# Optimization experiments

Hardware: AMD Instinct MI355X
Metric: run time of the kernel (lower is better)

## Reference

```python
import jax, jax.numpy as jnp
import numpy as np

B, N, K, H = 8, 4096, 16, 64
EPS_LN = 1e-5
EPS_STD = 1e-5


def _ln(x, g, b):
    m = jnp.mean(x, -1, keepdims=True)
    v = jnp.mean((x - m) ** 2, -1, keepdims=True)
    return (x - m) * jax.lax.rsqrt(v + EPS_LN) * g + b


def _res_block(x, W1, b1, g1, be1, W2, b2, g2, be2):
    h = jax.nn.relu(_ln(x @ W1 + b1, g1, be1))
    return jax.nn.relu(x + _ln(h @ W2 + b2, g2, be2))


def setup_inputs() -> dict:
    key = jax.random.key(0)
    ks = jax.random.split(key, 12)
    def w(k, shape, scale=0.02):
        return (jax.random.normal(k, shape) * scale).astype(jnp.float32)
    h = H
    z = jnp.zeros
    o = jnp.ones
    return dict(
        xyz=jax.random.normal(ks[0], (B, N, 3), jnp.float32),
        x=jax.random.normal(ks[1], (B, N, 3), jnp.float32),
        W_emb=w(ks[2], (3, h)), b_emb=z(h), g_emb=o(h), be_emb=z(h),
        alpha=o(h), beta=z(h),
        W_pre=w(ks[3], (2 * h, 4 * h)), b_pre=z(4 * h), g_pre=o(4 * h), be_pre=z(4 * h),
        W1a=w(ks[4], (4 * h, 8 * h)), b1a=z(8 * h), g1a=o(8 * h), be1a=z(8 * h),
        W2a=w(ks[5], (8 * h, 4 * h)), b2a=z(4 * h), g2a=o(4 * h), be2a=z(4 * h),
        W_pos=w(ks[6], (4 * h, 4 * h)), b_pos=z(4 * h), g_pos=o(4 * h), be_pos=z(4 * h),
        W1b=w(ks[7], (4 * h, 8 * h)), b1b=z(8 * h), g1b=o(8 * h), be1b=z(8 * h),
        W2b=w(ks[8], (8 * h, 4 * h)), b2b=z(4 * h), g2b=o(4 * h), be2b=z(4 * h),
        W_fin=w(ks[9], (4 * h, h)), b_fin=z(h), g_fin=o(h), be_fin=z(h),
    )


def _forward(xyz, x, W_emb, b_emb, g_emb, be_emb, alpha, beta,
             W_pre, b_pre, g_pre, be_pre,
             W1a, b1a, g1a, be1a, W2a, b2a, g2a, be2a,
             W_pos, b_pos, g_pos, be_pos,
             W1b, b1b, g1b, be1b, W2b, b2b, g2b, be2b,
             W_fin, b_fin, g_fin, be_fin):
    # embedding: Linear + LN + ReLU  -> [B, N, H]
    pts = jax.nn.relu(_ln(x @ W_emb + b_emb, g_emb, be_emb))
    # KNN over xyz (squared distances, smallest K)
    sq = jnp.sum(xyz ** 2, -1)                                   # [B, N]
    sqd = sq[:, :, None] + sq[:, None, :] - 2.0 * jnp.einsum('bnd,bmd->bnm', xyz, xyz)
    _, idx = jax.lax.top_k(-sqd, K)                              # [B, N, K]
    grouped = jax.vmap(lambda p, i: p[i])(pts, idx)              # [B, N, K, H]
    # anchor normalization: mean = center feature; std over whole per-batch flattened diff (ddof=1)
    diff = grouped - pts[:, :, None, :]
    std = jnp.std(diff.reshape(diff.shape[0], -1), axis=-1, ddof=1)[:, None, None, None]
    grouped = diff / (std + EPS_STD) * alpha + beta
    newp = jnp.concatenate(
        [grouped, jnp.broadcast_to(pts[:, :, None, :], grouped.shape)], axis=-1)  # [B, N, K, 2H]
    # pre MLP + residual block, then max-pool over K
    y = _ln(newp @ W_pre + b_pre, g_pre, be_pre)                 # [B, N, K, 4H]
    y = _res_block(y, W1a, b1a, g1a, be1a, W2a, b2a, g2a, be2a)
    y = jnp.max(y, axis=2)                                       # [B, N, 4H]
    # pos MLP + residual block, then max-pool over N
    y = _ln(y @ W_pos + b_pos, g_pos, be_pos)
    y = _res_block(y, W1b, b1b, g1b, be1b, W2b, b2b, g2b, be2b)
    y = jnp.max(y, axis=1)                                       # [B, 4H]
    return _ln(y @ W_fin + b_fin, g_fin, be_fin)                 # [B, H]


def reference(xyz, x, W_emb, b_emb, g_emb, be_emb, alpha, beta,
              W_pre, b_pre, g_pre, be_pre,
              W1a, b1a, g1a, be1a, W2a, b2a, g2a, be2a,
              W_pos, b_pos, g_pos, be_pos,
              W1b, b1b, g1b, be1b, W2b, b2b, g2b, be2b,
              W_fin, b_fin, g_fin, be_fin):
    return _forward(xyz, x, W_emb, b_emb, g_emb, be_emb, alpha, beta,
                    W_pre, b_pre, g_pre, be_pre,
                    W1a, b1a, g1a, be1a, W2a, b2a, g2a, be2a,
                    W_pos, b_pos, g_pos, be_pos,
                    W1b, b1b, g1b, be1b, W2b, b2b, g2b, be2b,
                    W_fin, b_fin, g_fin, be_fin)
```

## Files before the change

kernel.cpp:

```cpp
#include <hip/hip_runtime.h>
#include <hip/hip_bf16.h>

typedef __bf16 bf16_t;
typedef __bf16 bf16x8 __attribute__((ext_vector_type(8)));
typedef __bf16 bf16x4 __attribute__((ext_vector_type(4)));
typedef float f32x4 __attribute__((ext_vector_type(4)));
typedef unsigned long long u64;

#define LNEPS 1e-5f
#define STDEPS 1e-5f

#define PTS_OFF   0UL
#define IDX_OFF   8519680UL
#define RED_OFF   10616832UL
#define STD_OFF   (RED_OFF + 128UL)
#define WP_OFF    10617088UL
#define POOL1_OFF 11862272UL
#define POOL2_OFF 28639488UL
#define WS_NEED   28647680UL

__global__ void k_pack(const float* __restrict__ W, bf16_t* __restrict__ Wp,
                       int No, int sh, int n)
{
  int i = blockIdx.x * 256 + threadIdx.x;
  if (i >= n) return;
  int j = i & 7;
  int l = (i >> 3) & 63;
  int rest = i >> 9;
  int kc = rest & ((1 << sh) - 1);
  int t = rest >> sh;
  int k = kc * 32 + (l >> 4) * 8 + j;
  int col = t * 16 + (l & 15);
  Wp[i] = (bf16_t)W[k * No + col];
}

__global__ void k_embed(const float* __restrict__ xyz, const float* __restrict__ x,
                        const float* __restrict__ W, const float* __restrict__ bb,
                        const float* __restrict__ g, const float* __restrict__ be,
                        float* __restrict__ pts, float4* __restrict__ cand4)
{
  int p = blockIdx.x * 256 + threadIdx.x;
  float x0 = x[p * 3 + 0], x1 = x[p * 3 + 1], x2 = x[p * 3 + 2];
  float e[64];
  float s = 0.f;
  #pragma unroll
  for (int j = 0; j < 64; ++j) {
    float v = bb[j];
    v = fmaf(x0, W[j], v);
    v = fmaf(x1, W[64 + j], v);
    v = fmaf(x2, W[128 + j], v);
    e[j] = v; s += v;
  }
  float mean = s * (1.f / 64.f);
  float vs = 0.f;
  #pragma unroll
  for (int j = 0; j < 64; ++j) { float d = e[j] - mean; vs = fmaf(d, d, vs); }
  float rstd = rsqrtf(vs * (1.f / 64.f) + LNEPS);
  #pragma unroll
  for (int j = 0; j < 64; ++j)
    pts[p * 64 + j] = fmaxf(0.f, (e[j] - mean) * rstd * g[j] + be[j]);
  float z0 = xyz[p * 3 + 0], z1 = xyz[p * 3 + 1], z2 = xyz[p * 3 + 2];
  cand4[p] = make_float4(z0, z1, z2, z0 * z0 + z1 * z1 + z2 * z2);
}

__device__ __forceinline__ void insert16(u64* a, u64 key)
{
  #pragma unroll
  for (int j = 15; j >= 1; --j) {
    u64 lo = (key < a[j - 1]) ? a[j - 1] : key;
    a[j] = (key < a[j]) ? lo : a[j];
  }
  a[0] = (key < a[0]) ? key : a[0];
}

__device__ __forceinline__ void merge16(u64* a, const u64* b)
{
  u64 m[16];
  #pragma unroll
  for (int i = 0; i < 16; ++i) m[i] = (a[i] < b[15 - i]) ? a[i] : b[15 - i];
  #pragma unroll
  for (int d = 8; d >= 1; d >>= 1) {
    #pragma unroll
    for (int i = 0; i < 16; ++i) {
      if ((i & d) == 0) {
        u64 xv = m[i], yv = m[i + d];
        bool c = yv < xv;
        m[i] = c ? yv : xv;
        m[i + d] = c ? xv : yv;
      }
    }
  }
  #pragma unroll
  for (int i = 0; i < 16; ++i) a[i] = m[i];
}

__global__ __launch_bounds__(256) void k_knn(const float4* __restrict__ cand4,
                                             int* __restrict__ idx)
{
  __shared__ u64 ldsB[256 * 17];
  const int tid = threadIdx.x;
  const int l = tid & 63;
  const int w = tid >> 6;
  const int wu = __builtin_amdgcn_readfirstlane(w);
  const int b = blockIdx.x >> 6;
  const int g = blockIdx.x & 63;
  const int p = (b << 12) + (g << 6) + l;
  const float4 q = cand4[p];
  const float4* __restrict__ cbase = cand4 + (b << 12) + (wu << 10);
  const int mbase = wu << 10;
  u64 arr[16];
  const u64 KINF = ((u64)0x7F800000u << 32) | 0xFFFFFFFFu;
  #pragma unroll
  for (int j = 0; j < 16; ++j) arr[j] = KINF;
  float tf = 3.4e38f;
  int cnt = 0;
  u64* myb = &ldsB[tid * 17];

  for (int m0 = 0; m0 < 1024; m0 += 8) {
    if (__any(cnt > 8)) {
      for (int j2 = 0; j2 < cnt; ++j2) insert16(arr, myb[j2]);
      cnt = 0;
      tf = __uint_as_float((unsigned)(arr[15] >> 32));
    }
    #pragma unroll
    for (int u = 0; u < 8; ++u) {
      float4 c = cbase[m0 + u];
      float dot = q.x * c.x;
      dot = fmaf(q.y, c.y, dot);
      dot = fmaf(q.z, c.z, dot);
      float d = fmaxf(fmaf(-2.f, dot, q.w + c.w), 0.f);
      if (d < tf) {
        myb[cnt] = ((u64)__float_as_uint(d) << 32) | (unsigned)(mbase + m0 + u);
        ++cnt;
      }
    }
  }
  for (int j2 = 0; j2 < cnt; ++j2) insert16(arr, myb[j2]);

  #pragma unroll
  for (int j = 0; j < 16; ++j) myb[j] = arr[j];
  __syncthreads();
  if ((w & 1) == 0) {
    u64 brr[16];
    #pragma unroll
    for (int j = 0; j < 16; ++j) brr[j] = ldsB[((w + 1) * 64 + l) * 17 + j];
    merge16(arr, brr);
    #pragma unroll
    for (int j = 0; j < 16; ++j) myb[j] = arr[j];
  }
  __syncthreads();
  if (w == 0) {
    u64 brr[16];
    #pragma unroll
    for (int j = 0; j < 16; ++j) brr[j] = ldsB[(2 * 64 + l) * 17 + j];
    merge16(arr, brr);
    #pragma unroll
    for (int j = 0; j < 16; ++j) idx[p * 16 + j] = (int)(unsigned)(arr[j] & 0xFFFFFFFFu);
  }
}

__global__ void k_stdred(const float* __restrict__ pts, const int* __restrict__ idx,
                         double* __restrict__ red)
{
  int b = blockIdx.x >> 6, chunk = blockIdx.x & 63;
  int tid = threadIdx.x;
  int h = tid & 63;
  int r0 = chunk * 1024 + (tid >> 6);
  float s = 0.f, s2 = 0.f;
  for (int i = 0; i < 256; ++i) {
    int row = r0 + 4 * i;
    int n = row >> 4, k = row & 15;
    int ni = idx[((b << 12) + n) * 16 + k];
    float v = pts[((b << 12) + ni) * 64 + h] - pts[((b << 12) + n) * 64 + h];
    s += v; s2 = fmaf(v, v, s2);
  }
  double ds = (double)s, ds2 = (double)s2;
  #pragma unroll
  for (int m = 1; m < 64; m <<= 1) {
    ds += __shfl_xor(ds, m, 64);
    ds2 += __shfl_xor(ds2, m, 64);
  }
  __shared__ double sred[8];
  int w = tid >> 6;
  if ((tid & 63) == 0) { sred[w] = ds; sred[4 + w] = ds2; }
  __syncthreads();
  if (tid == 0) {
    atomicAdd(&red[b], sred[0] + sred[1] + sred[2] + sred[3]);
    atomicAdd(&red[8 + b], sred[4] + sred[5] + sred[6] + sred[7]);
  }
}

__global__ void k_stdfin(const double* __restrict__ red, float* __restrict__ stdv)
{
  int t = threadIdx.x;
  if (t < 8) {
    double M = 4194304.0;
    double s = red[t], s2 = red[8 + t];
    double var = (s2 - s * s / M) / (M - 1.0);
    stdv[t] = (float)sqrt(var);
  }
}

__device__ __forceinline__ bf16x4 cvt4(f32x4 v)
{
  bf16x4 o;
  o[0] = (bf16_t)v[0]; o[1] = (bf16_t)v[1]; o[2] = (bf16_t)v[2]; o[3] = (bf16_t)v[3];
  return o;
}

__device__ __forceinline__ f32x4 shflmax(f32x4 v, int m)
{
  f32x4 r;
  #pragma unroll
  for (int c = 0; c < 4; ++c) r[c] = fmaxf(v[c], __shfl_xor(v[c], m, 64));
  return r;
}

template <int NKC, int NTW>
__device__ __forceinline__ void gemm_sw(const bf16_t* __restrict__ inS, const int instride,
                                        const bf16_t* __restrict__ Wp,
                                        const int w, const int l, f32x4 (*acc)[4])
{
  const int lr = l & 15, lg = l >> 4;
  const bf16x8* __restrict__ Wf = (const bf16x8*)Wp;
  #pragma unroll
  for (int kc = 0; kc < NKC; ++kc) {
    bf16x8 af[4];
    #pragma unroll
    for (int rt = 0; rt < 4; ++rt)
      af[rt] = *(const bf16x8*)(inS + (rt * 16 + lr) * instride + kc * 32 + lg * 8);
    #pragma unroll
    for (int ct = 0; ct < NTW; ++ct) {
      bf16x8 bw = Wf[((w * NTW + ct) * NKC + kc) * 64 + l];
      #pragma unroll
      for (int rt = 0; rt < 4; ++rt)
        acc[ct][rt] = __builtin_amdgcn_mfma_f32_16x16x32_bf16(bw, af[rt], acc[ct][rt], 0, 0, 0);
    }
  }
}

template <int NTW>
__device__ __forceinline__ void add_bias_stats(f32x4 (*acc)[4], const float* __restrict__ bias,
                                               const int w, const int l,
                                               float* __restrict__ smP, float* __restrict__ sqP)
{
  const int lr = l & 15, lg = l >> 4;
  float sm[4] = {0.f, 0.f, 0.f, 0.f}, sq[4] = {0.f, 0.f, 0.f, 0.f};
  #pragma unroll
  for (int ct = 0; ct < NTW; ++ct) {
    const int t = w * NTW + ct;
    f32x4 b4 = *(const f32x4*)(bias + t * 16 + 4 * lg);
    #pragma unroll
    for (int rt = 0; rt < 4; ++rt) {
      f32x4 v = acc[ct][rt] + b4;
      acc[ct][rt] = v;
      #pragma unroll
      for (int rg = 0; rg < 4; ++rg) { sm[rt] += v[rg]; sq[rt] = fmaf(v[rg], v[rg], sq[rt]); }
    }
  }
  #pragma unroll
  for (int rt = 0; rt < 4; ++rt) {
    sm[rt] += __shfl_xor(sm[rt], 16, 64); sq[rt] += __shfl_xor(sq[rt], 16, 64);
    sm[rt] += __shfl_xor(sm[rt], 32, 64); sq[rt] += __shfl_xor(sq[rt], 32, 64);
  }
  if (lg == 0) {
    #pragma unroll
    for (int rt = 0; rt < 4; ++rt) {
      smP[w * 64 + rt * 16 + lr] = sm[rt];
      sqP[w * 64 + rt * 16 + lr] = sq[rt];
    }
  }
}

__device__ __forceinline__ void mean_rstd(const float* __restrict__ smP,
                                          const float* __restrict__ sqP,
                                          const int lr, const float invNC,
                                          float* mean, float* rstd)
{
  #pragma unroll
  for (int rt = 0; rt < 4; ++rt) {
    int row = rt * 16 + lr;
    float s = 0.f, q = 0.f;
    #pragma unroll
    for (int u = 0; u < 8; ++u) { s += smP[u * 64 + row]; q += sqP[u * 64 + row]; }
    float me = s * invNC;
    float var = q * invNC - me * me;
    mean[rt] = me; rstd[rt] = rsqrtf(var + LNEPS);
  }
}

template <int NKCIN, int INSTRIDE, int REGEL, bool KPOOL>
__global__ __launch_bounds__(512, 4) void k_mlp(
    const float* __restrict__ pts, const int* __restrict__ idxp,
    const float* __restrict__ stdv, const float* __restrict__ alpha,
    const float* __restrict__ beta, const bf16_t* __restrict__ pooled1_in,
    const bf16_t* __restrict__ Wp0, const float* __restrict__ b0,
    const float* __restrict__ g0, const float* __restrict__ be0,
    const bf16_t* __restrict__ Wp1, const float* __restrict__ b1,
    const float* __restrict__ g1, const float* __restrict__ be1,
    const bf16_t* __restrict__ Wp2, const float* __restrict__ b2,
    const float* __restrict__ g2, const float* __restrict__ be2,
    bf16_t* __restrict__ pooled1_out, unsigned* __restrict__ pooled2)
{
  __shared__ bf16_t region[REGEL];
  __shared__ float smP[8 * 64];
  __shared__ float sqP[8 * 64];
  bf16_t* inS = region;
  bf16_t* yS = region + 64 * INSTRIDE;
  bf16_t* hS = region;

  const int tid = threadIdx.x;
  const int l = tid & 63, w = tid >> 6;
  const int lr = l & 15, lg = l >> 4;
  const int p0 = blockIdx.x * (KPOOL ? 4 : 64);
  const int bb = p0 >> 12;

  {
    const int r = tid >> 3, q = tid & 7;
    if (KPOOL) {
      const float inv = 1.0f / (stdv[bb] + STDEPS);
      const int p = p0 + (r >> 4), k = r & 15;
      if (q < 4) {
        const int ni = idxp[p * 16 + k];
        const float* sn = pts + ((size_t)(bb << 12) + ni) * 64 + q * 16;
        const float* sp = pts + (size_t)p * 64 + q * 16;
        #pragma unroll
        for (int i = 0; i < 4; ++i) {
          f32x4 a = *(const f32x4*)(sn + 4 * i);
          f32x4 c = *(const f32x4*)(sp + 4 * i);
          f32x4 av = *(const f32x4*)(alpha + q * 16 + 4 * i);
          f32x4 bv = *(const f32x4*)(beta + q * 16 + 4 * i);
          f32x4 v = (a - c) * (av * inv) + bv;
          *(bf16x4*)(inS + r * INSTRIDE + q * 16 + 4 * i) = cvt4(v);
        }
      } else {
        const float* sp = pts + (size_t)p * 64 + (q - 4) * 16;
        #pragma unroll
        for (int i = 0; i < 4; ++i) {
          f32x4 c = *(const f32x4*)(sp + 4 * i);
          *(bf16x4*)(inS + r * INSTRIDE + 64 + (q - 4) * 16 + 4 * i) = cvt4(c);
        }
      }
    } else {
      #pragma unroll
      for (int j = 0; j < 4; ++j) {
        *(bf16x8*)(inS + r * INSTRIDE + q * 32 + j * 8) =
            *(const bf16x8*)(pooled1_in + (size_t)(p0 + r) * 256 + q * 32 + j * 8);
      }
    }
  }
  __syncthreads();

  bf16x4 residb[2][4];
  float mean[4], rstd[4];

  {
    f32x4 acc[2][4];
    #pragma unroll
    for (int ct = 0; ct < 2; ++ct)
      #pragma unroll
      for (int rt = 0; rt < 4; ++rt) acc[ct][rt] = {0.f, 0.f, 0.f, 0.f};
    gemm_sw<NKCIN, 2>(inS, INSTRIDE, Wp0, w, l, acc);
    add_bias_stats<2>(acc, b0, w, l, smP, sqP);
    __syncthreads();
    mean_rstd(smP, sqP, lr, 1.f / 256.f, mean, rstd);
    #pragma unroll
    for (int ct = 0; ct < 2; ++ct) {
      const int t = w * 2 + ct;
      f32x4 g4 = *(const f32x4*)(g0 + t * 16 + 4 * lg);
      f32x4 be4 = *(const f32x4*)(be0 + t * 16 + 4 * lg);
      #pragma unroll
      for (int rt = 0; rt < 4; ++rt) {
        f32x4 v;
        #pragma unroll
        for (int rg = 0; rg < 4; ++rg)
          v[rg] = (acc[ct][rt][rg] - mean[rt]) * rstd[rt] * g4[rg] + be4[rg];
        bf16x4 vb = cvt4(v);
        residb[ct][rt] = vb;
        *(bf16x4*)(yS + (rt * 16 + lr) * 264 + t * 16 + 4 * lg) = vb;
      }
    }
  }
  __syncthreads();

  {
    f32x4 acc[4][4];
    #pragma unroll
    for (int ct = 0; ct < 4; ++ct)
      #pragma unroll
      for (int rt = 0; rt < 4; ++rt) acc[ct][rt] = {0.f, 0.f, 0.f, 0.f};
    gemm_sw<8, 4>(yS, 264, Wp1, w, l, acc);
    add_bias_stats<4>(acc, b1, w, l, smP, sqP);
    __syncthreads();
    mean_rstd(smP, sqP, lr, 1.f / 512.f, mean, rstd);
    #pragma unroll
    for (int ct = 0; ct < 4; ++ct) {
      const int t = w * 4 + ct;
      f32x4 g4 = *(const f32x4*)(g1 + t * 16 + 4 * lg);
      f32x4 be4 = *(const f32x4*)(be1 + t * 16 + 4 * lg);
      #pragma unroll
      for (int rt = 0; rt < 4; ++rt) {
        f32x4 v;
        #pragma unroll
        for (int rg = 0; rg < 4; ++rg)
          v[rg] = fmaxf(0.f, (acc[ct][rt][rg] - mean[rt]) * rstd[rt] * g4[rg] + be4[rg]);
        *(bf16x4*)(hS + (rt * 16 + lr) * 520 + t * 16 + 4 * lg) = cvt4(v);
      }
    }
  }
  __syncthreads();

  {
    f32x4 acc[2][4];
    #pragma unroll
    for (int ct = 0; ct < 2; ++ct)
      #pragma unroll
      for (int rt = 0; rt < 4; ++rt) acc[ct][rt] = {0.f, 0.f, 0.f, 0.f};
    gemm_sw<16, 2>(hS, 520, Wp2, w, l, acc);
    add_bias_stats<2>(acc, b2, w, l, smP, sqP);
    __syncthreads();
    mean_rstd(smP, sqP, lr, 1.f / 256.f, mean, rstd);
    #pragma unroll
    for (int ct = 0; ct < 2; ++ct) {
      const int t = w * 2 + ct;
      f32x4 g4 = *(const f32x4*)(g2 + t * 16 + 4 * lg);
      f32x4 be4 = *(const f32x4*)(be2 + t * 16 + 4 * lg);
      f32x4 mv = {0.f, 0.f, 0.f, 0.f};
      #pragma unroll
      for (int rt = 0; rt < 4; ++rt) {
        f32x4 v;
        #pragma unroll
        for (int rg = 0; rg < 4; ++rg)
          v[rg] = fmaxf(0.f, (float)residb[ct][rt][rg] +
                             (acc[ct][rt][rg] - mean[rt]) * rstd[rt] * g4[rg] + be4[rg]);
        if (KPOOL) {
          v = shflmax(v, 1); v = shflmax(v, 2); v = shflmax(v, 4); v = shflmax(v, 8);
          if (lr == 0)
            *(bf16x4*)(pooled1_out + (size_t)(p0 + rt) * 256 + t * 16 + 4 * lg) = cvt4(v);
        } else {
          #pragma unroll
          for (int rg = 0; rg < 4; ++rg) mv[rg] = fmaxf(mv[rg], v[rg]);
        }
      }
      if (!KPOOL) {
        mv = shflmax(mv, 1); mv = shflmax(mv, 2); mv = shflmax(mv, 4); mv = shflmax(mv, 8);
        if (lr == 0) {
          #pragma unroll
          for (int rg = 0; rg < 4; ++rg)
            atomicMax(&pooled2[bb * 256 + t * 16 + 4 * lg + rg], __float_as_uint(mv[rg]));
        }
      }
    }
  }
}

__global__ void k_final(const unsigned* __restrict__ pooled2,
                        const float* __restrict__ W, const float* __restrict__ bb,
                        const float* __restrict__ g, const float* __restrict__ be,
                        float* __restrict__ out)
{
  int w = threadIdx.x >> 6;
  int l = threadIdx.x & 63;
  float acc = bb[l];
  for (int k = 0; k < 256; ++k)
    acc = fmaf(__uint_as_float(pooled2[w * 256 + k]), W[k * 64 + l], acc);
  float sm = acc, sq = acc * acc;
  #pragma unroll
  for (int m = 1; m < 64; m <<= 1) {
    sm += __shfl_xor(sm, m, 64);
    sq += __shfl_xor(sq, m, 64);
  }
  float mean = sm * (1.f / 64.f);
  float var = sq * (1.f / 64.f) - mean * mean;
  out[w * 64 + l] = (acc - mean) * rsqrtf(var + LNEPS) * g[l] + be[l];
}

extern "C" void kernel_launch(void* const* d_in, const int* in_sizes, int n_in,
                              void* d_out, int out_size, void* d_ws, size_t ws_size,
                              hipStream_t stream)
{
  if (ws_size < WS_NEED) return;
  const float* xyz = (const float*)d_in[0];
  const float* x = (const float*)d_in[1];
  const float* W_emb = (const float*)d_in[2];
  const float* b_emb = (const float*)d_in[3];
  const float* g_emb = (const float*)d_in[4];
  const float* be_emb = (const float*)d_in[5];
  const float* alpha = (const float*)d_in[6];
  const float* beta = (const float*)d_in[7];
  const float* W_pre = (const float*)d_in[8];
  const float* b_pre = (const float*)d_in[9];
  const float* g_pre = (const float*)d_in[10];
  const float* be_pre = (const float*)d_in[11];
  const float* W1a = (const float*)d_in[12];
  const float* b1a = (const float*)d_in[13];
  const float* g1a = (const float*)d_in[14];
  const float* be1a = (const float*)d_in[15];
  const float* W2a = (const float*)d_in[16];
  const float* b2a = (const float*)d_in[17];
  const float* g2a = (const float*)d_in[18];
  const float* be2a = (const float*)d_in[19];
  const float* W_pos = (const float*)d_in[20];
  const float* b_pos = (const float*)d_in[21];
  const float* g_pos = (const float*)d_in[22];
  const float* be_pos = (const float*)d_in[23];
  const float* W1b = (const float*)d_in[24];
  const float* b1b = (const float*)d_in[25];
  const float* g1b = (const float*)d_in[26];
  const float* be1b = (const float*)d_in[27];
  const float* W2b = (const float*)d_in[28];
  const float* b2b = (const float*)d_in[29];
  const float* g2b = (const float*)d_in[30];
  const float* be2b = (const float*)d_in[31];
  const float* W_fin = (const float*)d_in[32];
  const float* b_fin = (const float*)d_in[33];
  const float* g_fin = (const float*)d_in[34];
  const float* be_fin = (const float*)d_in[35];

  char* ws = (char*)d_ws;
  float* pts = (float*)(ws + PTS_OFF);
  int* idx = (int*)(ws + IDX_OFF);
  double* red = (double*)(ws + RED_OFF);
  float* stdv = (float*)(ws + STD_OFF);
  bf16_t* WpPre = (bf16_t*)(ws + WP_OFF);
  bf16_t* Wp1a = WpPre + 32768;
  bf16_t* Wp2a = Wp1a + 131072;
  bf16_t* WpPos = Wp2a + 131072;
  bf16_t* Wp1b = WpPos + 65536;
  bf16_t* Wp2b = Wp1b + 131072;
  bf16_t* pooled1 = (bf16_t*)(ws + POOL1_OFF);
  float4* cand4 = (float4*)(ws + POOL1_OFF);
  unsigned* pooled2 = (unsigned*)(ws + POOL2_OFF);

  hipMemsetAsync(ws + RED_OFF, 0, 256, stream);
  hipMemsetAsync(ws + POOL2_OFF, 0, 8192, stream);

  k_pack<<<32768 / 256, 256, 0, stream>>>(W_pre, WpPre, 256, 2, 32768);
  k_pack<<<131072 / 256, 256, 0, stream>>>(W1a, Wp1a, 512, 3, 131072);
  k_pack<<<131072 / 256, 256, 0, stream>>>(W2a, Wp2a, 256, 4, 131072);
  k_pack<<<65536 / 256, 256, 0, stream>>>(W_pos, WpPos, 256, 3, 65536);
  k_pack<<<131072 / 256, 256, 0, stream>>>(W1b, Wp1b, 512, 3, 131072);
  k_pack<<<131072 / 256, 256, 0, stream>>>(W2b, Wp2b, 256, 4, 131072);

  k_embed<<<32768 / 256, 256, 0, stream>>>(xyz, x, W_emb, b_emb, g_emb, be_emb, pts, cand4);
  k_knn<<<512, 256, 0, stream>>>(cand4, idx);
  k_stdred<<<512, 256, 0, stream>>>(pts, idx, red);
  k_stdfin<<<1, 64, 0, stream>>>(red, stdv);

  k_mlp<4, 136, 33280, true><<<8192, 512, 0, stream>>>(
      pts, idx, stdv, alpha, beta, nullptr,
      WpPre, b_pre, g_pre, be_pre,
      Wp1a, b1a, g1a, be1a,
      Wp2a, b2a, g2a, be2a,
      pooled1, nullptr);
  k_mlp<8, 264, 33792, false><<<512, 512, 0, stream>>>(
      nullptr, nullptr, nullptr, nullptr, nullptr, pooled1,
      WpPos, b_pos, g_pos, be_pos,
      Wp1b, b1b, g1b, be1b,
      Wp2b, b2b, g2b, be2b,
      nullptr, pooled2);
  k_final<<<1, 512, 0, stream>>>(pooled2, W_fin, b_fin, g_fin, be_fin, (float*)d_out);
}
```

Baseline: 1.005 ms.

## Split middle GEMM into column chunks and stash first chunk in LDS

The 256->512 GEMM in the MLP kernel now runs in two parts, first one 16-column tile and then three, instead of holding all four tiles' accumulators at once. The first tile's biased pre-LN output is converted to bf16 and stashed in shared memory, then read back after the LayerNorm statistics are known. The aim is to lower peak accumulator register pressure so the kernel avoids spills or keeps its 4-blocks-per-CU occupancy. In exchange it adds an extra barrier, LDS traffic, a second pass over the A fragments, and bf16 rounding of that tile before normalization.

```diff
diff --git a/kernel.cpp b/kernel.cpp
--- a/kernel.cpp
+++ b/kernel.cpp
@@ -219,7 +219,7 @@
 template <int NKC, int NTW>
 __device__ __forceinline__ void gemm_sw(const bf16_t* __restrict__ inS, const int instride,
                                         const bf16_t* __restrict__ Wp,
-                                        const int w, const int l, f32x4 (*acc)[4])
+                                        const int t0, const int l, f32x4 (*acc)[4])
 {
   const int lr = l & 15, lg = l >> 4;
   const bf16x8* __restrict__ Wf = (const bf16x8*)Wp;
@@ -231,7 +231,7 @@
       af[rt] = *(const bf16x8*)(inS + (rt * 16 + lr) * instride + kc * 32 + lg * 8);
     #pragma unroll
     for (int ct = 0; ct < NTW; ++ct) {
-      bf16x8 bw = Wf[((w * NTW + ct) * NKC + kc) * 64 + l];
+      bf16x8 bw = Wf[((t0 + ct) * NKC + kc) * 64 + l];
       #pragma unroll
       for (int rt = 0; rt < 4; ++rt)
         acc[ct][rt] = __builtin_amdgcn_mfma_f32_16x16x32_bf16(bw, af[rt], acc[ct][rt], 0, 0, 0);
@@ -240,16 +240,13 @@
 }
 
 template <int NTW>
-__device__ __forceinline__ void add_bias_stats(f32x4 (*acc)[4], const float* __restrict__ bias,
-                                               const int w, const int l,
-                                               float* __restrict__ smP, float* __restrict__ sqP)
-{
-  const int lr = l & 15, lg = l >> 4;
-  float sm[4] = {0.f, 0.f, 0.f, 0.f}, sq[4] = {0.f, 0.f, 0.f, 0.f};
+__device__ __forceinline__ void add_bias_acc(f32x4 (*acc)[4], const float* __restrict__ bias,
+                                             const int t0, const int lg,
+                                             float* sm, float* sq)
+{
   #pragma unroll
   for (int ct = 0; ct < NTW; ++ct) {
-    const int t = w * NTW + ct;
-    f32x4 b4 = *(const f32x4*)(bias + t * 16 + 4 * lg);
+    f32x4 b4 = *(const f32x4*)(bias + (t0 + ct) * 16 + 4 * lg);
     #pragma unroll
     for (int rt = 0; rt < 4; ++rt) {
       f32x4 v = acc[ct][rt] + b4;
@@ -258,6 +255,12 @@
       for (int rg = 0; rg < 4; ++rg) { sm[rt] += v[rg]; sq[rt] = fmaf(v[rg], v[rg], sq[rt]); }
     }
   }
+}
+
+__device__ __forceinline__ void stats_store(float* sm, float* sq, const int w, const int l,
+                                            float* __restrict__ smP, float* __restrict__ sqP)
+{
+  const int lr = l & 15, lg = l >> 4;
   #pragma unroll
   for (int rt = 0; rt < 4; ++rt) {
     sm[rt] += __shfl_xor(sm[rt], 16, 64); sq[rt] += __shfl_xor(sq[rt], 16, 64);
@@ -308,6 +311,7 @@
   bf16_t* inS = region;
   bf16_t* yS = region + 64 * INSTRIDE;
   bf16_t* hS = region;
+  bf16_t* stashS = region;
 
   const int tid = threadIdx.x;
   const int l = tid & 63, w = tid >> 6;
@@ -360,8 +364,10 @@
     for (int ct = 0; ct < 2; ++ct)
       #pragma unroll
       for (int rt = 0; rt < 4; ++rt) acc[ct][rt] = {0.f, 0.f, 0.f, 0.f};
-    gemm_sw<NKCIN, 2>(inS, INSTRIDE, Wp0, w, l, acc);
-    add_bias_stats<2>(acc, b0, w, l, smP, sqP);
+    gemm_sw<NKCIN, 2>(inS, INSTRIDE, Wp0, w * 2, l, acc);
+    float sm[4] = {0.f, 0.f, 0.f, 0.f}, sq[4] = {0.f, 0.f, 0.f, 0.f};
+    add_bias_acc<2>(acc, b0, w * 2, lg, sm, sq);
+    stats_store(sm, sq, w, l, smP, sqP);
     __syncthreads();
     mean_rstd(smP, sqP, lr, 1.f / 256.f, mean, rstd);
     #pragma unroll
@@ -384,18 +390,35 @@
   __syncthreads();
 
   {
-    f32x4 acc[4][4];
-    #pragma unroll
-    for (int ct = 0; ct < 4; ++ct)
-      #pragma unroll
-      for (int rt = 0; rt < 4; ++rt) acc[ct][rt] = {0.f, 0.f, 0.f, 0.f};
-    gemm_sw<8, 4>(yS, 264, Wp1, w, l, acc);
-    add_bias_stats<4>(acc, b1, w, l, smP, sqP);
+    float sm[4] = {0.f, 0.f, 0.f, 0.f}, sq[4] = {0.f, 0.f, 0.f, 0.f};
+    {
+      f32x4 accA[1][4];
+      #pragma unroll
+      for (int rt = 0; rt < 4; ++rt) accA[0][rt] = {0.f, 0.f, 0.f, 0.f};
+      gemm_sw<8, 1>(yS, 264, Wp1, w * 4, l, accA);
+      add_bias_acc<1>(accA, b1, w * 4, lg, sm, sq);
+      #pragma unroll
+      for (int rt = 0; rt < 4; ++rt)
+        *(bf16x4*)(stashS + w * 1024 + (rt * 16 + lr) * 16 + 4 * lg) = cvt4(accA[0][rt]);
+    }
+    f32x4 accB[3][4];
+    #pragma unroll
+    for (int ct = 0; ct < 3; ++ct)
+      #pragma unroll
+      for (int rt = 0; rt < 4; ++rt) accB[ct][rt] = {0.f, 0.f, 0.f, 0.f};
+    gemm_sw<8, 3>(yS, 264, Wp1, w * 4 + 1, l, accB);
+    add_bias_acc<3>(accB, b1, w * 4 + 1, lg, sm, sq);
+    stats_store(sm, sq, w, l, smP, sqP);
     __syncthreads();
     mean_rstd(smP, sqP, lr, 1.f / 512.f, mean, rstd);
-    #pragma unroll
-    for (int ct = 0; ct < 4; ++ct) {
-      const int t = w * 4 + ct;
+    bf16x4 sA[4];
+    #pragma unroll
+    for (int rt = 0; rt < 4; ++rt)
+      sA[rt] = *(const bf16x4*)(stashS + w * 1024 + (rt * 16 + lr) * 16 + 4 * lg);
+    __syncthreads();
+    #pragma unroll
+    for (int ct = 0; ct < 3; ++ct) {
+      const int t = w * 4 + 1 + ct;
       f32x4 g4 = *(const f32x4*)(g1 + t * 16 + 4 * lg);
       f32x4 be4 = *(const f32x4*)(be1 + t * 16 + 4 * lg);
       #pragma unroll
@@ -403,7 +426,20 @@
         f32x4 v;
         #pragma unroll
         for (int rg = 0; rg < 4; ++rg)
-          v[rg] = fmaxf(0.f, (acc[ct][rt][rg] - mean[rt]) * rstd[rt] * g4[rg] + be4[rg]);
+          v[rg] = fmaxf(0.f, (accB[ct][rt][rg] - mean[rt]) * rstd[rt] * g4[rg] + be4[rg]);
+        *(bf16x4*)(hS + (rt * 16 + lr) * 520 + t * 16 + 4 * lg) = cvt4(v);
+      }
+    }
+    {
+      const int t = w * 4;
+      f32x4 g4 = *(const f32x4*)(g1 + t * 16 + 4 * lg);
+      f32x4 be4 = *(const f32x4*)(be1 + t * 16 + 4 * lg);
+      #pragma unroll
+      for (int rt = 0; rt < 4; ++rt) {
+        f32x4 v;
+        #pragma unroll
+        for (int rg = 0; rg < 4; ++rg)
+          v[rg] = fmaxf(0.f, ((float)sA[rt][rg] - mean[rt]) * rstd[rt] * g4[rg] + be4[rg]);
         *(bf16x4*)(hS + (rt * 16 + lr) * 520 + t * 16 + 4 * lg) = cvt4(v);
       }
     }
@@ -416,8 +452,10 @@
     for (int ct = 0; ct < 2; ++ct)
       #pragma unroll
       for (int rt = 0; rt < 4; ++rt) acc[ct][rt] = {0.f, 0.f, 0.f, 0.f};
-    gemm_sw<16, 2>(hS, 520, Wp2, w, l, acc);
-    add_bias_stats<2>(acc, b2, w, l, smP, sqP);
+    gemm_sw<16, 2>(hS, 520, Wp2, w * 2, l, acc);
+    float sm[4] = {0.f, 0.f, 0.f, 0.f}, sq[4] = {0.f, 0.f, 0.f, 0.f};
+    add_bias_acc<2>(acc, b2, w * 2, lg, sm, sq);
+    stats_store(sm, sq, w, l, smP, sqP);
     __syncthreads();
     mean_rstd(smP, sqP, lr, 1.f / 256.f, mean, rstd);
     #pragma unroll
```

Measured after the change: 943.5 us. 6.1% less time.

## Double wavefronts per MLP block to 16, halving column tiles per wave

Applied to the files above, without the earlier changes.

Both fused MLP kernels now launch 1024-thread blocks (16 waves) instead of 512, and each wave computes half as many 16-column output tiles in every GEMM stage. LayerNorm partial-stat buffers grow to 16 slots, and the stat helper is split into a bias-accumulate step and a shuffle/store step. The aim is more waves per block to hide MFMA and LDS latency and to cut accumulator registers per thread. In exchange, each wave reloads the shared A fragments for fewer MFMAs, and the larger blocks may limit how many blocks fit per CU.

```diff
diff --git a/kernel.cpp b/kernel.cpp
--- a/kernel.cpp
+++ b/kernel.cpp
@@ -219,7 +219,7 @@
 template <int NKC, int NTW>
 __device__ __forceinline__ void gemm_sw(const bf16_t* __restrict__ inS, const int instride,
                                         const bf16_t* __restrict__ Wp,
-                                        const int w, const int l, f32x4 (*acc)[4])
+                                        const int t0, const int l, f32x4 (*acc)[4])
 {
   const int lr = l & 15, lg = l >> 4;
   const bf16x8* __restrict__ Wf = (const bf16x8*)Wp;
@@ -231,7 +231,7 @@
       af[rt] = *(const bf16x8*)(inS + (rt * 16 + lr) * instride + kc * 32 + lg * 8);
     #pragma unroll
     for (int ct = 0; ct < NTW; ++ct) {
-      bf16x8 bw = Wf[((w * NTW + ct) * NKC + kc) * 64 + l];
+      bf16x8 bw = Wf[((t0 + ct) * NKC + kc) * 64 + l];
       #pragma unroll
       for (int rt = 0; rt < 4; ++rt)
         acc[ct][rt] = __builtin_amdgcn_mfma_f32_16x16x32_bf16(bw, af[rt], acc[ct][rt], 0, 0, 0);
@@ -240,16 +240,13 @@
 }
 
 template <int NTW>
-__device__ __forceinline__ void add_bias_stats(f32x4 (*acc)[4], const float* __restrict__ bias,
-                                               const int w, const int l,
-                                               float* __restrict__ smP, float* __restrict__ sqP)
-{
-  const int lr = l & 15, lg = l >> 4;
-  float sm[4] = {0.f, 0.f, 0.f, 0.f}, sq[4] = {0.f, 0.f, 0.f, 0.f};
+__device__ __forceinline__ void add_bias_acc(f32x4 (*acc)[4], const float* __restrict__ bias,
+                                             const int t0, const int lg,
+                                             float* sm, float* sq)
+{
   #pragma unroll
   for (int ct = 0; ct < NTW; ++ct) {
-    const int t = w * NTW + ct;
-    f32x4 b4 = *(const f32x4*)(bias + t * 16 + 4 * lg);
+    f32x4 b4 = *(const f32x4*)(bias + (t0 + ct) * 16 + 4 * lg);
     #pragma unroll
     for (int rt = 0; rt < 4; ++rt) {
       f32x4 v = acc[ct][rt] + b4;
@@ -258,6 +255,12 @@
       for (int rg = 0; rg < 4; ++rg) { sm[rt] += v[rg]; sq[rt] = fmaf(v[rg], v[rg], sq[rt]); }
     }
   }
+}
+
+__device__ __forceinline__ void stats_store(float* sm, float* sq, const int w, const int l,
+                                            float* __restrict__ smP, float* __restrict__ sqP)
+{
+  const int lr = l & 15, lg = l >> 4;
   #pragma unroll
   for (int rt = 0; rt < 4; ++rt) {
     sm[rt] += __shfl_xor(sm[rt], 16, 64); sq[rt] += __shfl_xor(sq[rt], 16, 64);
@@ -282,7 +285,7 @@
     int row = rt * 16 + lr;
     float s = 0.f, q = 0.f;
     #pragma unroll
-    for (int u = 0; u < 8; ++u) { s += smP[u * 64 + row]; q += sqP[u * 64 + row]; }
+    for (int u = 0; u < 16; ++u) { s += smP[u * 64 + row]; q += sqP[u * 64 + row]; }
     float me = s * invNC;
     float var = q * invNC - me * me;
     mean[rt] = me; rstd[rt] = rsqrtf(var + LNEPS);
@@ -290,7 +293,7 @@
 }
 
 template <int NKCIN, int INSTRIDE, int REGEL, bool KPOOL>
-__global__ __launch_bounds__(512, 4) void k_mlp(
+__global__ __launch_bounds__(1024, 4) void k_mlp(
     const float* __restrict__ pts, const int* __restrict__ idxp,
     const float* __restrict__ stdv, const float* __restrict__ alpha,
     const float* __restrict__ beta, const bf16_t* __restrict__ pooled1_in,
@@ -303,8 +306,8 @@
     bf16_t* __restrict__ pooled1_out, unsigned* __restrict__ pooled2)
 {
   __shared__ bf16_t region[REGEL];
-  __shared__ float smP[8 * 64];
-  __shared__ float sqP[8 * 64];
+  __shared__ float smP[16 * 64];
+  __shared__ float sqP[16 * 64];
   bf16_t* inS = region;
   bf16_t* yS = region + 64 * INSTRIDE;
   bf16_t* hS = region;
@@ -316,86 +319,87 @@
   const int bb = p0 >> 12;
 
   {
-    const int r = tid >> 3, q = tid & 7;
+    const int r = tid >> 4, q = tid & 15;
     if (KPOOL) {
       const float inv = 1.0f / (stdv[bb] + STDEPS);
       const int p = p0 + (r >> 4), k = r & 15;
-      if (q < 4) {
+      if (q < 8) {
         const int ni = idxp[p * 16 + k];
-        const float* sn = pts + ((size_t)(bb << 12) + ni) * 64 + q * 16;
-        const float* sp = pts + (size_t)p * 64 + q * 16;
+        const float* sn = pts + ((size_t)(bb << 12) + ni) * 64 + q * 8;
+        const float* sp = pts + (size_t)p * 64 + q * 8;
         #pragma unroll
-        for (int i = 0; i < 4; ++i) {
+        for (int i = 0; i < 2; ++i) {
           f32x4 a = *(const f32x4*)(sn + 4 * i);
           f32x4 c = *(const f32x4*)(sp + 4 * i);
-          f32x4 av = *(const f32x4*)(alpha + q * 16 + 4 * i);
-          f32x4 bv = *(const f32x4*)(beta + q * 16 + 4 * i);
+          f32x4 av = *(const f32x4*)(alpha + q * 8 + 4 * i);
+          f32x4 bv = *(const f32x4*)(beta + q * 8 + 4 * i);
           f32x4 v = (a - c) * (av * inv) + bv;
-          *(bf16x4*)(inS + r * INSTRIDE + q * 16 + 4 * i) = cvt4(v);
+          *(bf16x4*)(inS + r * INSTRIDE + q * 8 + 4 * i) = cvt4(v);
         }
       } else {
-        const float* sp = pts + (size_t)p * 64 + (q - 4) * 16;
+        const int qq = q - 8;
+        const float* sp = pts + (size_t)p * 64 + qq * 8;
         #pragma unroll
-        for (int i = 0; i < 4; ++i) {
+        for (int i = 0; i < 2; ++i) {
           f32x4 c = *(const f32x4*)(sp + 4 * i);
-          *(bf16x4*)(inS + r * INSTRIDE + 64 + (q - 4) * 16 + 4 * i) = cvt4(c);
+          *(bf16x4*)(inS + r * INSTRIDE + 64 + qq * 8 + 4 * i) = cvt4(c);
         }
       }
     } else {
       #pragma unroll
-      for (int j = 0; j < 4; ++j) {
-        *(bf16x8*)(inS + r * INSTRIDE + q * 32 + j * 8) =
-            *(const bf16x8*)(pooled1_in + (size_t)(p0 + r) * 256 + q * 32 + j * 8);
+      for (int j = 0; j < 2; ++j) {
+        *(bf16x8*)(inS + r * INSTRIDE + q * 16 + j * 8) =
+            *(const bf16x8*)(pooled1_in + (size_t)(p0 + r) * 256 + q * 16 + j * 8);
       }
     }
   }
   __syncthreads();
 
-  bf16x4 residb[2][4];
+  bf16x4 residb[4];
   float mean[4], rstd[4];
 
   {
-    f32x4 acc[2][4];
-    #pragma unroll
-    for (int ct = 0; ct < 2; ++ct)
-      #pragma unroll
-      for (int rt = 0; rt < 4; ++rt) acc[ct][rt] = {0.f, 0.f, 0.f, 0.f};
-    gemm_sw<NKCIN, 2>(inS, INSTRIDE, Wp0, w, l, acc);
-    add_bias_stats<2>(acc, b0, w, l, smP, sqP);
+    f32x4 acc[1][4];
+    #pragma unroll
+    for (int rt = 0; rt < 4; ++rt) acc[0][rt] = {0.f, 0.f, 0.f, 0.f};
+    gemm_sw<NKCIN, 1>(inS, INSTRIDE, Wp0, w, l, acc);
+    float sm[4] = {0.f, 0.f, 0.f, 0.f}, sq[4] = {0.f, 0.f, 0.f, 0.f};
+    add_bias_acc<1>(acc, b0, w, lg, sm, sq);
+    stats_store(sm, sq, w, l, smP, sqP);
     __syncthreads();
     mean_rstd(smP, sqP, lr, 1.f / 256.f, mean, rstd);
-    #pragma unroll
-    for (int ct = 0; ct < 2; ++ct) {
-      const int t = w * 2 + ct;
-      f32x4 g4 = *(const f32x4*)(g0 + t * 16 + 4 * lg);
-      f32x4 be4 = *(const f32x4*)(be0 + t * 16 + 4 * lg);
+    {
+      f32x4 g4 = *(const f32x4*)(g0 + w * 16 + 4 * lg);
+      f32x4 be4 = *(const f32x4*)(be0 + w * 16 + 4 * lg);
       #pragma unroll
       for (int rt = 0; rt < 4; ++rt) {
         f32x4 v;
         #pragma unroll
         for (int rg = 0; rg < 4; ++rg)
-          v[rg] = (acc[ct][rt][rg] - mean[rt]) * rstd[rt] * g4[rg] + be4[rg];
+          v[rg] = (acc[0][rt][rg] - mean[rt]) * rstd[rt] * g4[rg] + be4[rg];
         bf16x4 vb = cvt4(v);
-        residb[ct][rt] = vb;
-        *(bf16x4*)(yS + (rt * 16 + lr) * 264 + t * 16 + 4 * lg) = vb;
+        residb[rt] = vb;
+        *(bf16x4*)(yS + (rt * 16 + lr) * 264 + w * 16 + 4 * lg) = vb;
       }
     }
   }
   __syncthreads();
 
   {
-    f32x4 acc[4][4];
-    #pragma unroll
-    for (int ct = 0; ct < 4; ++ct)
+    f32x4 acc[2][4];
+    #pragma unroll
+    for (int ct = 0; ct < 2; ++ct)
       #pragma unroll
       for (int rt = 0; rt < 4; ++rt) acc[ct][rt] = {0.f, 0.f, 0.f, 0.f};
-    gemm_sw<8, 4>(yS, 264, Wp1, w, l, acc);
-    add_bias_stats<4>(acc, b1, w, l, smP, sqP);
+    gemm_sw<8, 2>(yS, 264, Wp1, w * 2, l, acc);
+    float sm[4] = {0.f, 0.f, 0.f, 0.f}, sq[4] = {0.f, 0.f, 0.f, 0.f};
+    add_bias_acc<2>(acc, b1, w * 2, lg, sm, sq);
+    stats_store(sm, sq, w, l, smP, sqP);
     __syncthreads();
     mean_rstd(smP, sqP, lr, 1.f / 512.f, mean, rstd);
     #pragma unroll
-    for (int ct = 0; ct < 4; ++ct) {
-      const int t = w * 4 + ct;
+    for (int ct = 0; ct < 2; ++ct) {
+      const int t = w * 2 + ct;
       f32x4 g4 = *(const f32x4*)(g1 + t * 16 + 4 * lg);
       f32x4 be4 = *(const f32x4*)(be1 + t * 16 + 4 * lg);
       #pragma unroll
@@ -411,32 +415,30 @@
   __syncthreads();
 
   {
-    f32x4 acc[2][4];
-    #pragma unroll
-    for (int ct = 0; ct < 2; ++ct)
-      #pragma unroll
-      for (int rt = 0; rt < 4; ++rt) acc[ct][rt] = {0.f, 0.f, 0.f, 0.f};
-    gemm_sw<16, 2>(hS, 520, Wp2, w, l, acc);
-    add_bias_stats<2>(acc, b2, w, l, smP, sqP);
+    f32x4 acc[1][4];
+    #pragma unroll
+    for (int rt = 0; rt < 4; ++rt) acc[0][rt] = {0.f, 0.f, 0.f, 0.f};
+    gemm_sw<16, 1>(hS, 520, Wp2, w, l, acc);
+    float sm[4] = {0.f, 0.f, 0.f, 0.f}, sq[4] = {0.f, 0.f, 0.f, 0.f};
+    add_bias_acc<1>(acc, b2, w, lg, sm, sq);
+    stats_store(sm, sq, w, l, smP, sqP);
     __syncthreads();
     mean_rstd(smP, sqP, lr, 1.f / 256.f, mean, rstd);
-    #pragma unroll
-    for (int ct = 0; ct < 2; ++ct) {
-      const int t = w * 2 + ct;
-      f32x4 g4 = *(const f32x4*)(g2 + t * 16 + 4 * lg);
-      f32x4 be4 = *(const f32x4*)(be2 + t * 16 + 4 * lg);
+    {
+      f32x4 g4 = *(const f32x4*)(g2 + w * 16 + 4 * lg);
+      f32x4 be4 = *(const f32x4*)(be2 + w * 16 + 4 * lg);
       f32x4 mv = {0.f, 0.f, 0.f, 0.f};
       #pragma unroll
       for (int rt = 0; rt < 4; ++rt) {
         f32x4 v;
         #pragma unroll
         for (int rg = 0; rg < 4; ++rg)
-          v[rg] = fmaxf(0.f, (float)residb[ct][rt][rg] +
-                             (acc[ct][rt][rg] - mean[rt]) * rstd[rt] * g4[rg] + be4[rg]);
+          v[rg] = fmaxf(0.f, (float)residb[rt][rg] +
+                             (acc[0][rt][rg] - mean[rt]) * rstd[rt] * g4[rg] + be4[rg]);
         if (KPOOL) {
           v = shflmax(v, 1); v = shflmax(v, 2); v = shflmax(v, 4); v = shflmax(v, 8);
           if (lr == 0)
-            *(bf16x4*)(pooled1_out + (size_t)(p0 + rt) * 256 + t * 16 + 4 * lg) = cvt4(v);
+            *(bf16x4*)(pooled1_out + (size_t)(p0 + rt) * 256 + w * 16 + 4 * lg) = cvt4(v);
         } else {
           #pragma unroll
           for (int rg = 0; rg < 4; ++rg) mv[rg] = fmaxf(mv[rg], v[rg]);
@@ -447,7 +449,7 @@
         if (lr == 0) {
           #pragma unroll
           for (int rg = 0; rg < 4; ++rg)
-            atomicMax(&pooled2[bb * 256 + t * 16 + 4 * lg + rg], __float_as_uint(mv[rg]));
+            atomicMax(&pooled2[bb * 256 + w * 16 + 4 * lg + rg], __float_as_uint(mv[rg]));
         }
       }
     }
@@ -547,13 +549,13 @@
   k_stdred<<<512, 256, 0, stream>>>(pts, idx, red);
   k_stdfin<<<1, 64, 0, stream>>>(red, stdv);
 
-  k_mlp<4, 136, 33280, true><<<8192, 512, 0, stream>>>(
+  k_mlp<4, 136, 33280, true><<<8192, 1024, 0, stream>>>(
       pts, idx, stdv, alpha, beta, nullptr,
       WpPre, b_pre, g_pre, be_pre,
       Wp1a, b1a, g1a, be1a,
       Wp2a, b2a, g2a, be2a,
       pooled1, nullptr);
-  k_mlp<8, 264, 33792, false><<<512, 512, 0, stream>>>(
+  k_mlp<8, 264, 33792, false><<<512, 1024, 0, stream>>>(
       nullptr, nullptr, nullptr, nullptr, nullptr, pooled1,
       WpPos, b_pos, g_pos, be_pos,
       Wp1b, b1b, g1b, be1b,
```

New measurement: 1.148 ms. 14.3% more time.
